# Kernel tuning notes

Measured on AMD Instinct MI355X. Metric: run time of the kernel, lower is better.

The kernel has to match this reference:

```python
import jax, jax.numpy as jnp
import numpy as np

C_IN = 128      # pair channel
C_HID = 32      # per-head hidden dim
H = 4           # heads
INF = 1e9
LN_EPS = 1e-5


def setup_inputs() -> dict:
    key = jax.random.key(0)
    ks = jax.random.split(key, 8)
    B, N = 1, 256
    s = 0.02
    return {
        "x": jax.random.normal(ks[0], (B, N, N, C_IN), dtype=jnp.float32),
        "mask": jnp.ones((B, N, N), dtype=jnp.float32),
        "ln_w": jnp.ones((C_IN,), dtype=jnp.float32),
        "ln_b": jnp.zeros((C_IN,), dtype=jnp.float32),
        "w_b": jax.random.normal(ks[1], (H, C_IN), dtype=jnp.float32) * s,      # triangle-bias linear (no bias)
        "w_q": jax.random.normal(ks[2], (H * C_HID, C_IN), dtype=jnp.float32) * s,
        "w_k": jax.random.normal(ks[3], (H * C_HID, C_IN), dtype=jnp.float32) * s,
        "w_v": jax.random.normal(ks[4], (H * C_HID, C_IN), dtype=jnp.float32) * s,
        "w_g": jax.random.normal(ks[5], (H * C_HID, C_IN), dtype=jnp.float32) * s,
        "b_g": jnp.ones((H * C_HID,), dtype=jnp.float32),
        "w_o": jax.random.normal(ks[6], (C_IN, H * C_HID), dtype=jnp.float32) * s,
        "b_o": jnp.zeros((C_IN,), dtype=jnp.float32),
    }


def reference(x, mask, ln_w, ln_b, w_b, w_q, w_k, w_v, w_g, b_g, w_o, b_o):
    # starting=True -> no transpose
    # LayerNorm over channel dim
    mu = jnp.mean(x, axis=-1, keepdims=True)
    var = jnp.var(x, axis=-1, keepdims=True)
    xn = (x - mu) * jax.lax.rsqrt(var + LN_EPS) * ln_w + ln_b            # [B,I,J,C]

    # mask bias: [B, I, 1, 1, J]
    mask_bias = (INF * (mask - 1.0))[..., :, None, None, :]

    # triangle bias: linear -> [B,I,J,H] -> permute -> [B,H,I,J] -> [B,1,H,I,J]
    tri_bias = jnp.einsum("bijc,hc->bhij", xn, w_b)[:, None]

    # QKV projections, per-head: weights reshaped to [H, D, C]
    Wq = w_q.reshape(H, C_HID, C_IN)
    Wk = w_k.reshape(H, C_HID, C_IN)
    Wv = w_v.reshape(H, C_HID, C_IN)
    scale = 1.0 / np.sqrt(C_HID)
    q = jnp.einsum("bijc,hdc->bihjd", xn, Wq) * scale                    # [B,I,H,J,D]
    k = jnp.einsum("bijc,hdc->bihjd", xn, Wk)
    v = jnp.einsum("bijc,hdc->bihjd", xn, Wv)

    # attention over the J (column) axis of each row i
    a = jnp.einsum("bihqd,bihkd->bihqk", q, k) + mask_bias + tri_bias    # [B,I,H,J,J]
    a = jax.nn.softmax(a, axis=-1)
    o = jnp.einsum("bihqk,bihkd->biqhd", a, v)                           # [B,I,J,H,D]

    # sigmoid gating
    g = jax.nn.sigmoid(jnp.einsum("bijc,ec->bije", xn, w_g) + b_g)       # [B,I,J,H*D]
    o = o.reshape(*o.shape[:-2], H * C_HID) * g

    # output projection
    return jnp.einsum("bije,ce->bijc", o, w_o) + b_o                     # [B,I,J,C_in]
```

## Files before the change

### kernel.cpp

```cpp
#include <hip/hip_runtime.h>

#define N 256
#define C 128
#define H 4
#define D 32
#define NP (N*N)
#define LN_EPS 1e-5f
#define LOG2E 1.4426950408889634f

using f32x4 = __attribute__((ext_vector_type(4))) float;
using bf8   = __attribute__((ext_vector_type(8))) short;

__device__ __forceinline__ float bf2f(ushort u) {
    union { uint u; float f; } v; v.u = ((uint)u) << 16; return v.f;
}
__device__ __forceinline__ ushort f2bf(float f) {
    union { float f; uint u; } v; v.f = f;
    uint u = v.u;
    u += 0x7fffu + ((u >> 16) & 1u);
    return (ushort)(u >> 16);
}
__device__ __forceinline__ ushort f2bf_trunc(float f) {
    union { float f; uint u; } v; v.f = f;
    return (ushort)(v.u >> 16);
}

__global__ __launch_bounds__(256) void prep_weights(
    const float* __restrict__ wq, const float* __restrict__ wk,
    const float* __restrict__ wv, const float* __restrict__ wg,
    const float* __restrict__ wb, const float* __restrict__ wo,
    ushort* __restrict__ Wcat, ushort* __restrict__ Wb, ushort* __restrict__ Wo)
{
    int t = blockIdx.x * 256 + threadIdx.x;
    const float scale = 0.17677669529663689f * LOG2E;
    float v;
    if (t < 16384)       v = wq[t] * scale;
    else if (t < 32768)  v = wk[t - 16384];
    else if (t < 49152)  v = wv[t - 32768];
    else                 v = wg[t - 49152];
    Wcat[t] = f2bf(v);
    if (t < 16384) Wo[t] = f2bf(wo[t]);
    if (t < 512)   Wb[t] = f2bf(wb[t]);
}

__global__ __launch_bounds__(256) void ln_kernel(
    const float* __restrict__ x, const float* __restrict__ lnw,
    const float* __restrict__ lnb, ushort* __restrict__ xn)
{
    int wave = threadIdx.x >> 6, lane = threadIdx.x & 63;
    int p = blockIdx.x * 4 + wave;
    const float* xp = x + (size_t)p * C;
    float a0 = xp[lane], a1 = xp[lane + 64];
    float s = a0 + a1, ss = a0 * a0 + a1 * a1;
    #pragma unroll
    for (int m = 1; m < 64; m <<= 1) {
        s  += __shfl_xor(s, m, 64);
        ss += __shfl_xor(ss, m, 64);
    }
    float mean = s * (1.f / 128.f);
    float var  = ss * (1.f / 128.f) - mean * mean;
    float rstd = rsqrtf(var + LN_EPS);
    ushort* op = xn + (size_t)p * C;
    op[lane]      = f2bf((a0 - mean) * rstd * lnw[lane]      + lnb[lane]);
    op[lane + 64] = f2bf((a1 - mean) * rstd * lnw[lane + 64] + lnb[lane + 64]);
}

__global__ __launch_bounds__(256) void tri_kernel(
    const ushort* __restrict__ xn, const ushort* __restrict__ Wb,
    ushort* __restrict__ tri_p)
{
    __shared__ float wb[512];
    int t = threadIdx.x;
    wb[t]       = bf2f(Wb[t]);
    wb[t + 256] = bf2f(Wb[t + 256]);
    __syncthreads();
    int p = blockIdx.x * 256 + t;
    const ushort* xp = xn + (size_t)p * C;
    float acc0 = 0, acc1 = 0, acc2 = 0, acc3 = 0;
    #pragma unroll
    for (int c8 = 0; c8 < 16; c8++) {
        uint4 pk = ((const uint4*)xp)[c8];
        const ushort* u = (const ushort*)&pk;
        #pragma unroll
        for (int j = 0; j < 8; j++) {
            float xv = bf2f(u[j]);
            int c = c8 * 8 + j;
            acc0 += xv * wb[c];
            acc1 += xv * wb[128 + c];
            acc2 += xv * wb[256 + c];
            acc3 += xv * wb[384 + c];
        }
    }
    int q = p >> 8, k = p & 255;
    int qc = q >> 4, quad = (q >> 2) & 3, r = q & 3;
    int n = k >> 4, lrow = k & 15;
    int lane = quad * 16 + lrow;
    int v = n * 4 + r, j = v >> 3, m = v & 7;
    int base = ((qc * 8 + j) * 64 + lane) * 8 + m;
    tri_p[base]             = f2bf(acc0 * LOG2E);
    tri_p[65536 + base]     = f2bf(acc1 * LOG2E);
    tri_p[2 * 65536 + base] = f2bf(acc2 * LOG2E);
    tri_p[3 * 65536 + base] = f2bf(acc3 * LOG2E);
}

__global__ __launch_bounds__(512, 4) void proj_gemm(
    const ushort* __restrict__ xn, const ushort* __restrict__ Wcat,
    const float* __restrict__ bg,
    ushort* __restrict__ qb, ushort* __restrict__ kb,
    ushort* __restrict__ vbT, ushort* __restrict__ gate)
{
    __shared__ ushort At[128 * 128];
    __shared__ ushort Bt[128 * 128];
    int mt = blockIdx.x;
    int nt = blockIdx.y;
    int t  = threadIdx.x;

    const uint4* Ag = (const uint4*)(xn   + (size_t)mt * 128 * C);
    const uint4* Bg = (const uint4*)(Wcat + (size_t)nt * 128 * C);
    #pragma unroll
    for (int ii = 0; ii < 4; ii++) {
        int idx = t + ii * 512;
        int row = idx >> 4, c8 = idx & 15;
        int sc = row * 16 + (c8 ^ (row & 7));
        ((uint4*)At)[sc] = Ag[idx];
        ((uint4*)Bt)[sc] = Bg[idx];
    }
    __syncthreads();

    int wave = t >> 6, lane = t & 63;
    int lrow = lane & 15, quad = lane >> 4;
    int wr = wave >> 1, wc = wave & 1;

    f32x4 acc[2][4];
    #pragma unroll
    for (int mi = 0; mi < 2; mi++)
        #pragma unroll
        for (int ni = 0; ni < 4; ni++) acc[mi][ni] = (f32x4){0.f, 0.f, 0.f, 0.f};

    #pragma unroll
    for (int ks = 0; ks < 4; ks++) {
        int c8 = ks * 4 + quad;
        bf8 a[2], b[4];
        #pragma unroll
        for (int mi = 0; mi < 2; mi++) {
            int row = wr * 32 + mi * 16 + lrow;
            a[mi] = *(const bf8*)&At[(row * 16 + (c8 ^ (row & 7))) * 8];
        }
        #pragma unroll
        for (int ni = 0; ni < 4; ni++) {
            int row = wc * 64 + ni * 16 + lrow;
            b[ni] = *(const bf8*)&Bt[(row * 16 + (c8 ^ (row & 7))) * 8];
        }
        #pragma unroll
        for (int mi = 0; mi < 2; mi++)
            #pragma unroll
            for (int ni = 0; ni < 4; ni++)
                acc[mi][ni] = __builtin_amdgcn_mfma_f32_16x16x32_bf16(a[mi], b[ni], acc[mi][ni], 0, 0, 0);
    }

    if (nt == 2) {
        __syncthreads();
        #pragma unroll
        for (int mi = 0; mi < 2; mi++) {
            #pragma unroll
            for (int ni = 0; ni < 4; ni++) {
                int col = wc * 64 + ni * 16 + lrow;
                #pragma unroll
                for (int r = 0; r < 4; r++) {
                    int keyl = wr * 32 + mi * 16 + quad * 4 + r;
                    Bt[col * 128 + (keyl ^ (lrow << 3))] = f2bf(acc[mi][ni][r]);
                }
            }
        }
        __syncthreads();
        int i_row = mt >> 1;
        #pragma unroll
        for (int itr = 0; itr < 4; itr++) {
            int oidx = itr * 512 + t;
            int col = oidx >> 4, kc = oidx & 15;
            bf8 val = *(const bf8*)&Bt[col * 128 + ((kc * 8) ^ ((col & 15) << 3))];
            *(bf8*)&vbT[(size_t)(i_row * 128 + col) * N + (mt & 1) * 128 + kc * 8] = val;
        }
    } else {
        ushort* dst = (nt == 0) ? qb : (nt == 1) ? kb : gate;
        bool gated = (nt == 3);
        #pragma unroll
        for (int mi = 0; mi < 2; mi++) {
            #pragma unroll
            for (int ni = 0; ni < 4; ni++) {
                int col = wc * 64 + ni * 16 + lrow;
                #pragma unroll
                for (int r = 0; r < 4; r++) {
                    int row = mt * 128 + wr * 32 + mi * 16 + quad * 4 + r;
                    float v = acc[mi][ni][r];
                    if (gated) v = 1.f / (1.f + __expf(-(v + bg[col])));
                    dst[(size_t)row * C + col] = f2bf(v);
                }
            }
        }
    }
}

__global__ __launch_bounds__(512, 4) void attn_kernel(
    const ushort* __restrict__ qb, const ushort* __restrict__ kb,
    const ushort* __restrict__ vbT, const ushort* __restrict__ tri_p,
    const float* __restrict__ mask, ushort* __restrict__ ob)
{
    __shared__ ushort Kf[8192];
    __shared__ ushort Vf[8192];
    __shared__ ushort Pf[8][2048];

    int i  = blockIdx.x;
    int h  = blockIdx.y;
    int t  = threadIdx.x;
    int wave = t >> 6, lane = t & 63;
    int lrow = lane & 15, quad = lane >> 4;

    {
        const ushort* kt = kb + (size_t)(i * N) * C + h * D;
        #pragma unroll
        for (int it = 0; it < 2; it++) {
            int idx = it * 512 + t;
            int key = idx >> 2, d0 = (idx & 3) * 8;
            bf8 kv = *(const bf8*)(kt + (size_t)key * C + d0);
            int c = (idx >> 6) * 64 + (idx & 3) * 16 + ((idx >> 2) & 15);
            *(bf8*)&Kf[c * 8] = kv;
        }
    }
    {
        const ushort* vt = vbT + (size_t)((i * H + h) * D) * N;
        #pragma unroll
        for (int it = 0; it < 2; it++) {
            int idx = it * 512 + t;
            bf8 vv = *(const bf8*)(vt + idx * 8);
            int c = (idx >> 9) * 512 + ((idx >> 2) & 7) * 64 + (idx & 3) * 16 + ((idx >> 5) & 15);
            c ^= (c >> 6) & 7;
            *(bf8*)&Vf[c * 8] = vv;
        }
    }
    float mb[16];
    #pragma unroll
    for (int n = 0; n < 16; n++)
        mb[n] = (1e9f * LOG2E) * (mask[i * N + n * 16 + lrow] - 1.0f);
    __syncthreads();

    ushort* Pw = &Pf[wave][0];
    const ushort* trih = tri_p + (size_t)h * 65536;
    int pq = quad * 32 + (lrow & 7);
    int l3 = (lrow >> 3) & 1;

    #pragma unroll 1
    for (int cc = 0; cc < 2; cc++) {
        int qc = wave * 2 + cc;
        bf8 aq = *(const bf8*)(qb + (size_t)(i * N + qc * 16 + lrow) * C + h * D + quad * 8);
        float sum[4] = {0.f, 0.f, 0.f, 0.f};
        f32x4 o[2];
        o[0] = (f32x4){0.f, 0.f, 0.f, 0.f};
        o[1] = (f32x4){0.f, 0.f, 0.f, 0.f};

        #pragma unroll
        for (int half = 0; half < 2; half++) {
            f32x4 s8[8];
            #pragma unroll
            for (int n8 = 0; n8 < 8; n8++) {
                bf8 kf = *(const bf8*)&Kf[((half * 8 + n8) * 64 + lane) * 8];
                s8[n8] = __builtin_amdgcn_mfma_f32_16x16x32_bf16(
                    aq, kf, (f32x4){0.f, 0.f, 0.f, 0.f}, 0, 0, 0);
            }
            const ushort* tp = trih + ((size_t)(qc * 8 + half * 4) * 64 + lane) * 8;
            bf8 tf[4];
            #pragma unroll
            for (int jj = 0; jj < 4; jj++)
                tf[jj] = *(const bf8*)(tp + jj * 512);

            #pragma unroll
            for (int n8 = 0; n8 < 8; n8++) {
                int pa = (n8 >> 1) * 512 + (((n8 << 1) + l3) & 3) * 128 + pq;
                #pragma unroll
                for (int r = 0; r < 4; r++) {
                    float tb = bf2f(((const ushort*)&tf[n8 >> 1])[((n8 & 1) << 2) + r]);
                    float e  = exp2f(s8[n8][r] + tb + mb[half * 8 + n8]);
                    sum[r]  += e;
                    Pw[pa + r * 8] = f2bf_trunc(e);
                }
            }
            __asm__ volatile("s_waitcnt lgkmcnt(0)" ::: "memory");

            #pragma unroll
            for (int ks = 0; ks < 4; ks++) {
                bf8 ap = *(const bf8*)&Pw[(ks * 64 + lane) * 8];
                int ksg = half * 4 + ks;
                #pragma unroll
                for (int nv = 0; nv < 2; nv++) {
                    int c = nv * 512 + ksg * 64 + (lane ^ (ksg & 7));
                    bf8 bv = *(const bf8*)&Vf[c * 8];
                    o[nv] = __builtin_amdgcn_mfma_f32_16x16x32_bf16(ap, bv, o[nv], 0, 0, 0);
                }
            }
        }
        #pragma unroll
        for (int r = 0; r < 4; r++) {
            float s = sum[r];
            s += __shfl_xor(s, 1, 64);
            s += __shfl_xor(s, 2, 64);
            s += __shfl_xor(s, 4, 64);
            s += __shfl_xor(s, 8, 64);
            sum[r] = 1.f / s;
        }
        #pragma unroll
        for (int nv = 0; nv < 2; nv++) {
            int d = nv * 16 + lrow;
            #pragma unroll
            for (int r = 0; r < 4; r++) {
                int qg = qc * 16 + quad * 4 + r;
                ob[(size_t)(i * N + qg) * C + h * D + d] = f2bf(o[nv][r] * sum[r]);
            }
        }
    }
}

__global__ __launch_bounds__(512, 4) void out_gemm(
    const ushort* __restrict__ ob, const ushort* __restrict__ gate,
    const ushort* __restrict__ Wo, const float* __restrict__ bo,
    float* __restrict__ out)
{
    __shared__ ushort At[128 * 128];
    __shared__ ushort Bt[128 * 128];
    int mt = blockIdx.x;
    int t  = threadIdx.x;

    const uint4* Og = (const uint4*)(ob   + (size_t)mt * 128 * C);
    const uint4* Gg = (const uint4*)(gate + (size_t)mt * 128 * C);
    const uint4* Bg = (const uint4*)Wo;
    #pragma unroll
    for (int ii = 0; ii < 4; ii++) {
        int idx = t + ii * 512;
        int row = idx >> 4, c8 = idx & 15;
        int sc = row * 16 + (c8 ^ (row & 7));
        uint4 o4 = Og[idx], g4 = Gg[idx], r4;
        const ushort* os = (const ushort*)&o4;
        const ushort* gs = (const ushort*)&g4;
        ushort* rs = (ushort*)&r4;
        #pragma unroll
        for (int j = 0; j < 8; j++) rs[j] = f2bf(bf2f(os[j]) * bf2f(gs[j]));
        ((uint4*)At)[sc] = r4;
        ((uint4*)Bt)[sc] = Bg[idx];
    }
    __syncthreads();

    int wave = t >> 6, lane = t & 63;
    int lrow = lane & 15, quad = lane >> 4;
    int wr = wave >> 1, wc = wave & 1;

    f32x4 acc[2][4];
    #pragma unroll
    for (int mi = 0; mi < 2; mi++)
        #pragma unroll
        for (int ni = 0; ni < 4; ni++) acc[mi][ni] = (f32x4){0.f, 0.f, 0.f, 0.f};

    #pragma unroll
    for (int ks = 0; ks < 4; ks++) {
        int c8 = ks * 4 + quad;
        bf8 a[2], b[4];
        #pragma unroll
        for (int mi = 0; mi < 2; mi++) {
            int row = wr * 32 + mi * 16 + lrow;
            a[mi] = *(const bf8*)&At[(row * 16 + (c8 ^ (row & 7))) * 8];
        }
        #pragma unroll
        for (int ni = 0; ni < 4; ni++) {
            int row = wc * 64 + ni * 16 + lrow;
            b[ni] = *(const bf8*)&Bt[(row * 16 + (c8 ^ (row & 7))) * 8];
        }
        #pragma unroll
        for (int mi = 0; mi < 2; mi++)
            #pragma unroll
            for (int ni = 0; ni < 4; ni++)
                acc[mi][ni] = __builtin_amdgcn_mfma_f32_16x16x32_bf16(a[mi], b[ni], acc[mi][ni], 0, 0, 0);
    }

    #pragma unroll
    for (int mi = 0; mi < 2; mi++) {
        #pragma unroll
        for (int ni = 0; ni < 4; ni++) {
            int col = wc * 64 + ni * 16 + lrow;
            float bias = bo[col];
            #pragma unroll
            for (int r = 0; r < 4; r++) {
                int row = mt * 128 + wr * 32 + mi * 16 + quad * 4 + r;
                out[(size_t)row * C + col] = acc[mi][ni][r] + bias;
            }
        }
    }
}

extern "C" void kernel_launch(void* const* d_in, const int* in_sizes, int n_in,
                              void* d_out, int out_size, void* d_ws, size_t ws_size,
                              hipStream_t stream)
{
    const float* x    = (const float*)d_in[0];
    const float* mask = (const float*)d_in[1];
    const float* lnw  = (const float*)d_in[2];
    const float* lnb  = (const float*)d_in[3];
    const float* wb   = (const float*)d_in[4];
    const float* wq   = (const float*)d_in[5];
    const float* wk   = (const float*)d_in[6];
    const float* wv   = (const float*)d_in[7];
    const float* wg   = (const float*)d_in[8];
    const float* bg   = (const float*)d_in[9];
    const float* wo   = (const float*)d_in[10];
    const float* bo   = (const float*)d_in[11];
    float* out = (float*)d_out;

    uintptr_t w = (uintptr_t)d_ws;
    ushort* xn    = (ushort*)w; w += (size_t)NP * C * 2;
    ushort* qb    = (ushort*)w; w += (size_t)NP * C * 2;
    ushort* kb    = (ushort*)w; w += (size_t)NP * C * 2;
    ushort* vbT   = (ushort*)w; w += (size_t)NP * C * 2;
    ushort* gate  = (ushort*)w; w += (size_t)NP * C * 2;
    ushort* ob    = (ushort*)w; w += (size_t)NP * C * 2;
    ushort* tri_p = (ushort*)w; w += (size_t)H * NP * 2;
    ushort* Wcat  = (ushort*)w; w += 512 * 128 * 2;
    ushort* Wb    = (ushort*)w; w += 512 * 2;
    ushort* Wo    = (ushort*)w; w += 128 * 128 * 2;

    prep_weights<<<256, 256, 0, stream>>>(wq, wk, wv, wg, wb, wo, Wcat, Wb, Wo);
    ln_kernel<<<NP / 4, 256, 0, stream>>>(x, lnw, lnb, xn);
    tri_kernel<<<NP / 256, 256, 0, stream>>>(xn, Wb, tri_p);
    proj_gemm<<<dim3(NP / 128, 4), 512, 0, stream>>>(xn, Wcat, bg, qb, kb, vbT, gate);
    attn_kernel<<<dim3(N, H), 512, 0, stream>>>(qb, kb, vbT, tri_p, mask, ob);
    out_gemm<<<NP / 128, 512, 0, stream>>>(ob, gate, Wo, bo, out);
}
```

Before: 181.2 us.

## Fuse LayerNorm, triangle bias and QKVG projection into one kernel

Merges the LayerNorm, triangle-bias and projection kernels into a single kernel. Each block normalizes its 128 rows straight into shared memory and computes the triangle bias with an MFMA against zero-padded Wb weights. It then loops over the four weight tiles, prefetching the next tile into registers. This removes the xn round trip through global memory, two launches, and the scalar tri computation. The cost is a grid cut from 2048 blocks to 512, each doing four times the GEMM work serially, which lowers parallelism.

```diff
diff --git a/kernel.cpp b/kernel.cpp
--- a/kernel.cpp
+++ b/kernel.cpp
@@ -10,6 +10,7 @@
 
 using f32x4 = __attribute__((ext_vector_type(4))) float;
 using bf8   = __attribute__((ext_vector_type(8))) short;
+using u16x4 = __attribute__((ext_vector_type(4))) unsigned short;
 
 __device__ __forceinline__ float bf2f(ushort u) {
     union { uint u; float f; } v; v.u = ((uint)u) << 16; return v.f;
@@ -29,7 +30,7 @@
     const float* __restrict__ wq, const float* __restrict__ wk,
     const float* __restrict__ wv, const float* __restrict__ wg,
     const float* __restrict__ wb, const float* __restrict__ wo,
-    ushort* __restrict__ Wcat, ushort* __restrict__ Wb, ushort* __restrict__ Wo)
+    ushort* __restrict__ Wcat, ushort* __restrict__ WbPad, ushort* __restrict__ Wo)
 {
     int t = blockIdx.x * 256 + threadIdx.x;
     const float scale = 0.17677669529663689f * LOG2E;
@@ -40,161 +41,179 @@
     else                 v = wg[t - 49152];
     Wcat[t] = f2bf(v);
     if (t < 16384) Wo[t] = f2bf(wo[t]);
-    if (t < 512)   Wb[t] = f2bf(wb[t]);
-}
-
-__global__ __launch_bounds__(256) void ln_kernel(
+    if (t < 2048)  WbPad[t] = (t < 512) ? f2bf(wb[t]) : (ushort)0;
+}
+
+__global__ __launch_bounds__(512, 4) void ln_proj(
     const float* __restrict__ x, const float* __restrict__ lnw,
-    const float* __restrict__ lnb, ushort* __restrict__ xn)
-{
-    int wave = threadIdx.x >> 6, lane = threadIdx.x & 63;
-    int p = blockIdx.x * 4 + wave;
-    const float* xp = x + (size_t)p * C;
-    float a0 = xp[lane], a1 = xp[lane + 64];
-    float s = a0 + a1, ss = a0 * a0 + a1 * a1;
-    #pragma unroll
-    for (int m = 1; m < 64; m <<= 1) {
-        s  += __shfl_xor(s, m, 64);
-        ss += __shfl_xor(ss, m, 64);
-    }
-    float mean = s * (1.f / 128.f);
-    float var  = ss * (1.f / 128.f) - mean * mean;
-    float rstd = rsqrtf(var + LN_EPS);
-    ushort* op = xn + (size_t)p * C;
-    op[lane]      = f2bf((a0 - mean) * rstd * lnw[lane]      + lnb[lane]);
-    op[lane + 64] = f2bf((a1 - mean) * rstd * lnw[lane + 64] + lnb[lane + 64]);
-}
-
-__global__ __launch_bounds__(256) void tri_kernel(
-    const ushort* __restrict__ xn, const ushort* __restrict__ Wb,
+    const float* __restrict__ lnb, const ushort* __restrict__ Wcat,
+    const ushort* __restrict__ WbPad, const float* __restrict__ bg,
+    ushort* __restrict__ qb, ushort* __restrict__ kb,
+    ushort* __restrict__ vbT, ushort* __restrict__ gate,
     ushort* __restrict__ tri_p)
-{
-    __shared__ float wb[512];
-    int t = threadIdx.x;
-    wb[t]       = bf2f(Wb[t]);
-    wb[t + 256] = bf2f(Wb[t + 256]);
-    __syncthreads();
-    int p = blockIdx.x * 256 + t;
-    const ushort* xp = xn + (size_t)p * C;
-    float acc0 = 0, acc1 = 0, acc2 = 0, acc3 = 0;
-    #pragma unroll
-    for (int c8 = 0; c8 < 16; c8++) {
-        uint4 pk = ((const uint4*)xp)[c8];
-        const ushort* u = (const ushort*)&pk;
-        #pragma unroll
-        for (int j = 0; j < 8; j++) {
-            float xv = bf2f(u[j]);
-            int c = c8 * 8 + j;
-            acc0 += xv * wb[c];
-            acc1 += xv * wb[128 + c];
-            acc2 += xv * wb[256 + c];
-            acc3 += xv * wb[384 + c];
-        }
-    }
-    int q = p >> 8, k = p & 255;
-    int qc = q >> 4, quad = (q >> 2) & 3, r = q & 3;
-    int n = k >> 4, lrow = k & 15;
-    int lane = quad * 16 + lrow;
-    int v = n * 4 + r, j = v >> 3, m = v & 7;
-    int base = ((qc * 8 + j) * 64 + lane) * 8 + m;
-    tri_p[base]             = f2bf(acc0 * LOG2E);
-    tri_p[65536 + base]     = f2bf(acc1 * LOG2E);
-    tri_p[2 * 65536 + base] = f2bf(acc2 * LOG2E);
-    tri_p[3 * 65536 + base] = f2bf(acc3 * LOG2E);
-}
-
-__global__ __launch_bounds__(512, 4) void proj_gemm(
-    const ushort* __restrict__ xn, const ushort* __restrict__ Wcat,
-    const float* __restrict__ bg,
-    ushort* __restrict__ qb, ushort* __restrict__ kb,
-    ushort* __restrict__ vbT, ushort* __restrict__ gate)
 {
     __shared__ ushort At[128 * 128];
     __shared__ ushort Bt[128 * 128];
     int mt = blockIdx.x;
-    int nt = blockIdx.y;
     int t  = threadIdx.x;
-
-    const uint4* Ag = (const uint4*)(xn   + (size_t)mt * 128 * C);
-    const uint4* Bg = (const uint4*)(Wcat + (size_t)nt * 128 * C);
-    #pragma unroll
-    for (int ii = 0; ii < 4; ii++) {
-        int idx = t + ii * 512;
-        int row = idx >> 4, c8 = idx & 15;
-        int sc = row * 16 + (c8 ^ (row & 7));
-        ((uint4*)At)[sc] = Ag[idx];
-        ((uint4*)Bt)[sc] = Bg[idx];
+    int wave = t >> 6, lane = t & 63;
+    int lane32 = lane & 31, rsel = lane >> 5;
+
+    {
+        const float4 w4 = ((const float4*)lnw)[lane32];
+        const float4 b4 = ((const float4*)lnb)[lane32];
+        const float* xb = x + (size_t)mt * 128 * C;
+        #pragma unroll
+        for (int pp = 0; pp < 8; pp++) {
+            int r = pp * 16 + wave * 2 + rsel;
+            float4 xv = ((const float4*)(xb + r * C))[lane32];
+            float s  = xv.x + xv.y + xv.z + xv.w;
+            float ss = xv.x*xv.x + xv.y*xv.y + xv.z*xv.z + xv.w*xv.w;
+            #pragma unroll
+            for (int m = 1; m < 32; m <<= 1) {
+                s  += __shfl_xor(s, m, 64);
+                ss += __shfl_xor(ss, m, 64);
+            }
+            float mean = s * (1.f / 128.f);
+            float var  = ss * (1.f / 128.f) - mean * mean;
+            float rstd = rsqrtf(var + LN_EPS);
+            u16x4 o;
+            o[0] = f2bf((xv.x - mean) * rstd * w4.x + b4.x);
+            o[1] = f2bf((xv.y - mean) * rstd * w4.y + b4.y);
+            o[2] = f2bf((xv.z - mean) * rstd * w4.z + b4.z);
+            o[3] = f2bf((xv.w - mean) * rstd * w4.w + b4.w);
+            int c8 = lane32 >> 1;
+            int chunk = r * 16 + (c8 ^ (r & 7));
+            *(u16x4*)&At[chunk * 8 + (lane32 & 1) * 4] = o;
+        }
     }
     __syncthreads();
 
-    int wave = t >> 6, lane = t & 63;
     int lrow = lane & 15, quad = lane >> 4;
     int wr = wave >> 1, wc = wave & 1;
 
-    f32x4 acc[2][4];
-    #pragma unroll
-    for (int mi = 0; mi < 2; mi++)
-        #pragma unroll
-        for (int ni = 0; ni < 4; ni++) acc[mi][ni] = (f32x4){0.f, 0.f, 0.f, 0.f};
-
+    bf8 afr[4][2];
     #pragma unroll
     for (int ks = 0; ks < 4; ks++) {
         int c8 = ks * 4 + quad;
-        bf8 a[2], b[4];
         #pragma unroll
         for (int mi = 0; mi < 2; mi++) {
             int row = wr * 32 + mi * 16 + lrow;
-            a[mi] = *(const bf8*)&At[(row * 16 + (c8 ^ (row & 7))) * 8];
-        }
-        #pragma unroll
-        for (int ni = 0; ni < 4; ni++) {
-            int row = wc * 64 + ni * 16 + lrow;
-            b[ni] = *(const bf8*)&Bt[(row * 16 + (c8 ^ (row & 7))) * 8];
-        }
+            afr[ks][mi] = *(const bf8*)&At[(row * 16 + (c8 ^ (row & 7))) * 8];
+        }
+    }
+
+    {
+        f32x4 at0 = (f32x4){0.f,0.f,0.f,0.f}, at1 = (f32x4){0.f,0.f,0.f,0.f};
+        #pragma unroll
+        for (int ks = 0; ks < 4; ks++) {
+            int c8 = ks * 4 + quad;
+            bf8 bt = *(const bf8*)(WbPad + lrow * C + c8 * 8);
+            at0 = __builtin_amdgcn_mfma_f32_16x16x32_bf16(afr[ks][0], bt, at0, 0, 0, 0);
+            at1 = __builtin_amdgcn_mfma_f32_16x16x32_bf16(afr[ks][1], bt, at1, 0, 0, 0);
+        }
+        if (wc == 0 && lrow < 4) {
+            int q = mt >> 1;
+            int qc = q >> 4, quadq = (q >> 2) & 3, rr = q & 3;
+            #pragma unroll
+            for (int mi = 0; mi < 2; mi++) {
+                #pragma unroll
+                for (int r = 0; r < 4; r++) {
+                    int k = (mt & 1) * 128 + wr * 32 + mi * 16 + quad * 4 + r;
+                    int n = k >> 4, lk = k & 15;
+                    int lanet = quadq * 16 + lk;
+                    int v = n * 4 + rr, j = v >> 3, m2 = v & 7;
+                    float val = (mi == 0) ? at0[r] : at1[r];
+                    tri_p[lrow * 65536 + ((qc * 8 + j) * 64 + lanet) * 8 + m2] =
+                        f2bf(val * LOG2E);
+                }
+            }
+        }
+    }
+
+    uint4 breg[4];
+    {
+        const uint4* Bg = (const uint4*)Wcat;
+        #pragma unroll
+        for (int ii = 0; ii < 4; ii++) breg[ii] = Bg[t + ii * 512];
+    }
+
+    #pragma unroll 1
+    for (int nt = 0; nt < 4; nt++) {
+        __syncthreads();
+        #pragma unroll
+        for (int ii = 0; ii < 4; ii++) {
+            int idx = t + ii * 512;
+            int row = idx >> 4, c8 = idx & 15;
+            ((uint4*)Bt)[row * 16 + (c8 ^ (row & 7))] = breg[ii];
+        }
+        __syncthreads();
+        if (nt < 3) {
+            const uint4* Bg = (const uint4*)(Wcat + (size_t)(nt + 1) * 128 * C);
+            #pragma unroll
+            for (int ii = 0; ii < 4; ii++) breg[ii] = Bg[t + ii * 512];
+        }
+
+        f32x4 acc[2][4];
         #pragma unroll
         for (int mi = 0; mi < 2; mi++)
             #pragma unroll
-            for (int ni = 0; ni < 4; ni++)
-                acc[mi][ni] = __builtin_amdgcn_mfma_f32_16x16x32_bf16(a[mi], b[ni], acc[mi][ni], 0, 0, 0);
-    }
-
-    if (nt == 2) {
-        __syncthreads();
-        #pragma unroll
-        for (int mi = 0; mi < 2; mi++) {
+            for (int ni = 0; ni < 4; ni++) acc[mi][ni] = (f32x4){0.f, 0.f, 0.f, 0.f};
+
+        #pragma unroll
+        for (int ks = 0; ks < 4; ks++) {
+            int c8 = ks * 4 + quad;
+            bf8 b[4];
             #pragma unroll
             for (int ni = 0; ni < 4; ni++) {
-                int col = wc * 64 + ni * 16 + lrow;
-                #pragma unroll
-                for (int r = 0; r < 4; r++) {
-                    int keyl = wr * 32 + mi * 16 + quad * 4 + r;
-                    Bt[col * 128 + (keyl ^ (lrow << 3))] = f2bf(acc[mi][ni][r]);
+                int row = wc * 64 + ni * 16 + lrow;
+                b[ni] = *(const bf8*)&Bt[(row * 16 + (c8 ^ (row & 7))) * 8];
+            }
+            #pragma unroll
+            for (int mi = 0; mi < 2; mi++)
+                #pragma unroll
+                for (int ni = 0; ni < 4; ni++)
+                    acc[mi][ni] = __builtin_amdgcn_mfma_f32_16x16x32_bf16(afr[ks][mi], b[ni], acc[mi][ni], 0, 0, 0);
+        }
+
+        if (nt == 2) {
+            __syncthreads();
+            #pragma unroll
+            for (int mi = 0; mi < 2; mi++) {
+                #pragma unroll
+                for (int ni = 0; ni < 4; ni++) {
+                    int col = wc * 64 + ni * 16 + lrow;
+                    #pragma unroll
+                    for (int r = 0; r < 4; r++) {
+                        int keyl = wr * 32 + mi * 16 + quad * 4 + r;
+                        Bt[col * 128 + (keyl ^ (lrow << 3))] = f2bf(acc[mi][ni][r]);
+                    }
                 }
             }
-        }
-        __syncthreads();
-        int i_row = mt >> 1;
-        #pragma unroll
-        for (int itr = 0; itr < 4; itr++) {
-            int oidx = itr * 512 + t;
-            int col = oidx >> 4, kc = oidx & 15;
-            bf8 val = *(const bf8*)&Bt[col * 128 + ((kc * 8) ^ ((col & 15) << 3))];
-            *(bf8*)&vbT[(size_t)(i_row * 128 + col) * N + (mt & 1) * 128 + kc * 8] = val;
-        }
-    } else {
-        ushort* dst = (nt == 0) ? qb : (nt == 1) ? kb : gate;
-        bool gated = (nt == 3);
-        #pragma unroll
-        for (int mi = 0; mi < 2; mi++) {
-            #pragma unroll
-            for (int ni = 0; ni < 4; ni++) {
-                int col = wc * 64 + ni * 16 + lrow;
-                #pragma unroll
-                for (int r = 0; r < 4; r++) {
-                    int row = mt * 128 + wr * 32 + mi * 16 + quad * 4 + r;
-                    float v = acc[mi][ni][r];
-                    if (gated) v = 1.f / (1.f + __expf(-(v + bg[col])));
-                    dst[(size_t)row * C + col] = f2bf(v);
+            __syncthreads();
+            int i_row = mt >> 1;
+            #pragma unroll
+            for (int itr = 0; itr < 4; itr++) {
+                int oidx = itr * 512 + t;
+                int col = oidx >> 4, kc = oidx & 15;
+                bf8 val = *(const bf8*)&Bt[col * 128 + ((kc * 8) ^ ((col & 15) << 3))];
+                *(bf8*)&vbT[(size_t)(i_row * 128 + col) * N + (mt & 1) * 128 + kc * 8] = val;
+            }
+        } else {
+            ushort* dst = (nt == 0) ? qb : (nt == 1) ? kb : gate;
+            bool gated = (nt == 3);
+            #pragma unroll
+            for (int mi = 0; mi < 2; mi++) {
+                #pragma unroll
+                for (int ni = 0; ni < 4; ni++) {
+                    int col = wc * 64 + ni * 16 + lrow;
+                    #pragma unroll
+                    for (int r = 0; r < 4; r++) {
+                        int row = mt * 128 + wr * 32 + mi * 16 + quad * 4 + r;
+                        float vv = acc[mi][ni][r];
+                        if (gated) vv = 1.f / (1.f + __expf(-(vv + bg[col])));
+                        dst[(size_t)row * C + col] = f2bf(vv);
+                    }
                 }
             }
         }
@@ -413,7 +432,6 @@
     float* out = (float*)d_out;
 
     uintptr_t w = (uintptr_t)d_ws;
-    ushort* xn    = (ushort*)w; w += (size_t)NP * C * 2;
     ushort* qb    = (ushort*)w; w += (size_t)NP * C * 2;
     ushort* kb    = (ushort*)w; w += (size_t)NP * C * 2;
     ushort* vbT   = (ushort*)w; w += (size_t)NP * C * 2;
@@ -421,13 +439,12 @@
     ushort* ob    = (ushort*)w; w += (size_t)NP * C * 2;
     ushort* tri_p = (ushort*)w; w += (size_t)H * NP * 2;
     ushort* Wcat  = (ushort*)w; w += 512 * 128 * 2;
-    ushort* Wb    = (ushort*)w; w += 512 * 2;
+    ushort* WbPad = (ushort*)w; w += 16 * 128 * 2;
     ushort* Wo    = (ushort*)w; w += 128 * 128 * 2;
 
-    prep_weights<<<256, 256, 0, stream>>>(wq, wk, wv, wg, wb, wo, Wcat, Wb, Wo);
-    ln_kernel<<<NP / 4, 256, 0, stream>>>(x, lnw, lnb, xn);
-    tri_kernel<<<NP / 256, 256, 0, stream>>>(xn, Wb, tri_p);
-    proj_gemm<<<dim3(NP / 128, 4), 512, 0, stream>>>(xn, Wcat, bg, qb, kb, vbT, gate);
+    prep_weights<<<256, 256, 0, stream>>>(wq, wk, wv, wg, wb, wo, Wcat, WbPad, Wo);
+    ln_proj<<<NP / 128, 512, 0, stream>>>(x, lnw, lnb, Wcat, WbPad, bg,
+                                          qb, kb, vbT, gate, tri_p);
     attn_kernel<<<dim3(N, H), 512, 0, stream>>>(qb, kb, vbT, tri_p, mask, ob);
     out_gemm<<<NP / 128, 512, 0, stream>>>(ob, gate, Wo, bo, out);
 }
```

Measured after the change: 199.5 us. 10.1% more time.
